# Kernel tuning notes

Measured on AMD Instinct MI355X. Metric: run time of the kernel, lower is better.

Reference implementation:

```python
import jax, jax.numpy as jnp
import numpy as np

B, T, D, H = 4, 2048, 384, 6
HD = D // H  # 64
HALF = HD // 2


def setup_inputs() -> dict:
    key = jax.random.key(0)
    k0, k1, k2 = jax.random.split(key, 3)
    x = jax.random.normal(k0, (B, T, D), jnp.float32)
    attn_bias = jnp.zeros((1, 1, T, T), jnp.float32)  # additive SDPA bias
    # standard RoPE tables: [T, HD/2]
    inv_freq = 1.0 / (10000.0 ** (np.arange(HALF, dtype=np.float32) / HALF))
    ang = np.arange(T, dtype=np.float32)[:, None] * inv_freq[None, :]
    cos = jnp.asarray(np.cos(ang), jnp.float32)
    sin = jnp.asarray(np.sin(ang), jnp.float32)
    w_qkv = jax.random.normal(k1, (D, 3 * D), jnp.float32) * (D ** -0.5)
    w_proj = jax.random.normal(k2, (D, D), jnp.float32) * (D ** -0.5)
    return {"x": x, "attn_bias": attn_bias, "cos": cos, "sin": sin,
            "w_qkv": w_qkv, "w_proj": w_proj}


def _apply_rope(x, cos, sin):
    # x: [b, h, t, hd]; cos/sin: [t, hd/2] -> rotate-half RoPE
    half = x.shape[-1] // 2
    x1, x2 = x[..., :half], x[..., half:]
    c = cos[None, None, :, :]
    s = sin[None, None, :, :]
    return jnp.concatenate([x1 * c - x2 * s, x2 * c + x1 * s], axis=-1)


def reference(x, attn_bias, cos, sin, w_qkv, w_proj):
    b, t, _ = x.shape
    qkv = (x @ w_qkv).reshape(b, t, 3, H, HD)  # fused QKV projection
    q = jnp.transpose(qkv[:, :, 0], (0, 2, 1, 3))  # [b,h,t,hd]
    k = jnp.transpose(qkv[:, :, 1], (0, 2, 1, 3))
    v = jnp.transpose(qkv[:, :, 2], (0, 2, 1, 3))
    q = _apply_rope(q, cos, sin)
    k = _apply_rope(k, cos, sin)
    scale = 1.0 / jnp.sqrt(jnp.asarray(HD, x.dtype))
    scores = jnp.einsum("bhqd,bhkd->bhqk", q, k) * scale + attn_bias
    attn = jax.nn.softmax(scores, axis=-1)
    out = jnp.einsum("bhqk,bhkd->bhqd", attn, v)
    out = jnp.transpose(out, (0, 2, 1, 3)).reshape(b, t, H * HD)
    return out @ w_proj
```

## Files before the change

### kernel.cpp

```cpp
#include <hip/hip_runtime.h>
#include <hip/hip_bf16.h>

#define BB   4
#define TT   2048
#define DDIM 384
#define HH   6
#define HD   64
#define BT   (BB*TT)
#define QKVC (3*DDIM)

typedef __attribute__((ext_vector_type(4))) short short4v;
typedef __attribute__((ext_vector_type(8))) short short8v;
typedef __attribute__((ext_vector_type(4))) float float4v;
typedef unsigned short u16;

static __device__ __forceinline__ u16 f2bu(float f) {
    __hip_bfloat16 h = __float2bfloat16(f);
    return __builtin_bit_cast(u16, h);
}

static __device__ __forceinline__ short8v ld_frag(const u16* p) {
    short4v a = *(const short4v*)p;
    short4v b = *(const short4v*)(p + 4);
    return __builtin_shufflevector(a, b, 0, 1, 2, 3, 4, 5, 6, 7);
}

static __device__ __forceinline__ void st8(u16* p, uint4 v) {
    *(uint2*)p       = make_uint2(v.x, v.y);
    *(uint2*)(p + 4) = make_uint2(v.z, v.w);
}

#define MFMA16(a, b, c) __builtin_amdgcn_mfma_f32_16x16x32_bf16((a), (b), (c), 0, 0, 0)

__global__ __launch_bounds__(256) void prep_kernel(
    const float* __restrict__ wqkv, const float* __restrict__ wproj,
    const float* __restrict__ x,
    u16* __restrict__ wqkvT, u16* __restrict__ wprojT, u16* __restrict__ xb)
{
    const int bid = blockIdx.x;
    const int t = threadIdx.x;
    if (bid >= 144) {
        size_t base = (size_t)(bid - 144) * 4096 + (size_t)t * 16;
        const float* gp = x + base;
        __align__(16) u16 tmp[16];
        #pragma unroll
        for (int u = 0; u < 4; ++u) {
            float4 v = *(const float4*)(gp + 4 * u);
            tmp[4 * u + 0] = f2bu(v.x); tmp[4 * u + 1] = f2bu(v.y);
            tmp[4 * u + 2] = f2bu(v.z); tmp[4 * u + 3] = f2bu(v.w);
        }
        *(uint4*)(xb + base)     = *(const uint4*)tmp;
        *(uint4*)(xb + base + 8) = *(const uint4*)(tmp + 8);
        return;
    }
    const float* in; u16* out; int K, C, c0, k0;
    if (bid < 108) { in = wqkv;  out = wqkvT;  K = DDIM; C = QKVC;
                     c0 = (bid % 18) * 64; k0 = (bid / 18) * 64; }
    else           { int b2 = bid - 108; in = wproj; out = wprojT; K = DDIM; C = DDIM;
                     c0 = (b2 % 6) * 64; k0 = (b2 / 6) * 64; }
    __shared__ float tr[64][65];
    {
        int kr = t >> 2, cb = (t & 3) * 16;
        const float* gp = in + (size_t)(k0 + kr) * C + c0 + cb;
        #pragma unroll
        for (int u = 0; u < 4; ++u) {
            float4 v = *(const float4*)(gp + 4 * u);
            tr[cb + 4 * u + 0][kr] = v.x;
            tr[cb + 4 * u + 1][kr] = v.y;
            tr[cb + 4 * u + 2][kr] = v.z;
            tr[cb + 4 * u + 3][kr] = v.w;
        }
    }
    __syncthreads();
    {
        int c = t >> 2, kb = (t & 3) * 16;
        __align__(16) u16 tmp[16];
        #pragma unroll
        for (int u = 0; u < 16; ++u) tmp[u] = f2bu(tr[c][kb + u]);
        u16* op = out + (size_t)(c0 + c) * K + k0 + kb;
        *(uint4*)op       = *(const uint4*)tmp;
        *(uint4*)(op + 8) = *(const uint4*)(tmp + 8);
    }
}

__global__ __launch_bounds__(256) void qkv_rope_kernel(
    const u16* __restrict__ xb, const u16* __restrict__ wt,
    const float* __restrict__ cs, const float* __restrict__ sn,
    u16* __restrict__ qb, u16* __restrict__ kb, u16* __restrict__ vtb)
{
    __shared__ __align__(16) u16 xs[2][64][68];
    __shared__ __align__(16) u16 ws[2][64][68];
    const int t = threadIdx.x;
    const int wv = t >> 6, lane = t & 63, quad = lane >> 4, lo = lane & 15;
    const int r0 = blockIdx.y * 64;
    const int c0 = blockIdx.x * 64;
    const int sr = t >> 3, sd = (t & 7) * 8;

    st8(&xs[0][sr][sd],      *(const uint4*)(xb + (size_t)(r0 + sr) * DDIM + sd));
    st8(&xs[0][sr + 32][sd], *(const uint4*)(xb + (size_t)(r0 + sr + 32) * DDIM + sd));
    st8(&ws[0][sr][sd],      *(const uint4*)(wt + (size_t)(c0 + sr) * DDIM + sd));
    st8(&ws[0][sr + 32][sd], *(const uint4*)(wt + (size_t)(c0 + sr + 32) * DDIM + sd));
    __syncthreads();

    float4v acc[4] = {};
    for (int kk = 0; kk < 6; ++kk) {
        const int cur = kk & 1, nxt = cur ^ 1;
        const int kkn = (kk < 5 ? kk + 1 : 5) * 64;
        uint4 xp0 = *(const uint4*)(xb + (size_t)(r0 + sr) * DDIM + kkn + sd);
        uint4 xp1 = *(const uint4*)(xb + (size_t)(r0 + sr + 32) * DDIM + kkn + sd);
        uint4 wp0 = *(const uint4*)(wt + (size_t)(c0 + sr) * DDIM + kkn + sd);
        uint4 wp1 = *(const uint4*)(wt + (size_t)(c0 + sr + 32) * DDIM + kkn + sd);

        #pragma unroll
        for (int kf = 0; kf < 2; ++kf) {
            short8v a = ld_frag(&xs[cur][16 * wv + lo][kf * 32 + quad * 8]);
            #pragma unroll
            for (int nt = 0; nt < 4; ++nt) {
                short8v b = ld_frag(&ws[cur][nt * 16 + lo][kf * 32 + quad * 8]);
                acc[nt] = MFMA16(a, b, acc[nt]);
            }
        }
        st8(&xs[nxt][sr][sd], xp0);
        st8(&xs[nxt][sr + 32][sd], xp1);
        st8(&ws[nxt][sr][sd], wp0);
        st8(&ws[nxt][sr + 32][sd], wp1);
        __syncthreads();
    }

    const int sec = blockIdx.x / 6;
    const int h   = blockIdx.x % 6;
    const int rbase = r0 + 16 * wv + 4 * quad;
    const int bidx  = r0 >> 11;
    const int tbase = rbase & (TT - 1);

    if (sec == 2) {
        #pragma unroll
        for (int nt = 0; nt < 4; ++nt) {
            int d = nt * 16 + lo;
            unsigned a0 = f2bu(acc[nt][0]) | ((unsigned)f2bu(acc[nt][1]) << 16);
            unsigned a1 = f2bu(acc[nt][2]) | ((unsigned)f2bu(acc[nt][3]) << 16);
            u16* gp = vtb + ((size_t)(bidx * HH + h) * HD + d) * TT + tbase;
            *(uint2*)gp = make_uint2(a0, a1);
        }
    } else {
        u16* dst = (sec == 0) ? qb : kb;
        #pragma unroll
        for (int np = 0; np < 2; ++np) {
            #pragma unroll
            for (int r = 0; r < 4; ++r) {
                int tpos = tbase + r;
                int ci = np * 16 + lo;
                float cv = cs[tpos * 32 + ci];
                float sv = sn[tpos * 32 + ci];
                float x1 = acc[np][r], x2 = acc[np + 2][r];
                u16* gp = dst + ((size_t)(bidx * HH + h) * TT + tpos) * HD;
                gp[ci]      = f2bu(x1 * cv - x2 * sv);
                gp[ci + 32] = f2bu(x2 * cv + x1 * sv);
            }
        }
    }
}

__global__ __launch_bounds__(256, 3) void attn_kernel(
    const u16* __restrict__ qb, const u16* __restrict__ kb, const u16* __restrict__ vtb,
    const float* __restrict__ bias, u16* __restrict__ ob)
{
    __shared__ __align__(16) u16 ks[2][64][68];
    __shared__ __align__(16) u16 vt[2][64][68];
    __shared__ __align__(16) u16 ps[4][16][72];

    const int t = threadIdx.x;
    const int wv = t >> 6, lane = t & 63, quad = lane >> 4, lo = lane & 15;
    const int bh = blockIdx.x;
    const int b = bh / HH, h = bh % HH;
    const int q0 = blockIdx.y * 64;
    const int qrow = q0 + 16 * wv + lo;

    const u16* qbase = qb + ((size_t)bh * TT + qrow) * HD + quad * 8;
    short8v aq0 = __builtin_bit_cast(short8v, *(const uint4*)qbase);
    short8v aq1 = __builtin_bit_cast(short8v, *(const uint4*)(qbase + 32));

    const int sr = t >> 3, sd = (t & 7) * 8;
    const u16* kbbase = kb + (size_t)bh * TT * HD;
    const u16* vtbase = vtb + (size_t)bh * HD * TT;
    const float* brow = bias + (size_t)qrow * TT + 4 * quad;

    st8(&ks[0][sr][sd],      *(const uint4*)(kbbase + (size_t)sr * HD + sd));
    st8(&ks[0][sr + 32][sd], *(const uint4*)(kbbase + (size_t)(sr + 32) * HD + sd));
    st8(&vt[0][sr][sd],      *(const uint4*)(vtbase + (size_t)sr * TT + sd));
    st8(&vt[0][sr + 32][sd], *(const uint4*)(vtbase + (size_t)(sr + 32) * TT + sd));
    float4 bcur[4];
    #pragma unroll
    for (int nt = 0; nt < 4; ++nt) bcur[nt] = *(const float4*)(brow + nt * 16);
    __syncthreads();

    float4v oacc[4] = {};
    float lacc[4] = {0.f, 0.f, 0.f, 0.f};

    for (int kt = 0; kt < TT / 64; ++kt) {
        const int cur = kt & 1, nxt = cur ^ 1;
        const int kn = (kt < 31 ? kt + 1 : 31) * 64;

        uint4 kp0 = *(const uint4*)(kbbase + (size_t)(kn + sr) * HD + sd);
        uint4 kp1 = *(const uint4*)(kbbase + (size_t)(kn + sr + 32) * HD + sd);
        uint4 vp0 = *(const uint4*)(vtbase + (size_t)sr * TT + kn + sd);
        uint4 vp1 = *(const uint4*)(vtbase + (size_t)(sr + 32) * TT + kn + sd);
        float4 bnxt[4];
        #pragma unroll
        for (int nt = 0; nt < 4; ++nt) bnxt[nt] = *(const float4*)(brow + kn + nt * 16);

        float4v s[4] = {};
        #pragma unroll
        for (int kf = 0; kf < 2; ++kf) {
            #pragma unroll
            for (int nt = 0; nt < 4; ++nt) {
                short8v kfr = ld_frag(&ks[cur][nt * 16 + lo][kf * 32 + quad * 8]);
                s[nt] = MFMA16(kfr, (kf ? aq1 : aq0), s[nt]);
            }
        }

        #pragma unroll
        for (int nt = 0; nt < 4; ++nt) {
            float p0 = __expf(fmaf(s[nt][0], 0.125f, bcur[nt].x));
            float p1 = __expf(fmaf(s[nt][1], 0.125f, bcur[nt].y));
            float p2 = __expf(fmaf(s[nt][2], 0.125f, bcur[nt].z));
            float p3 = __expf(fmaf(s[nt][3], 0.125f, bcur[nt].w));
            lacc[nt] += (p0 + p1) + (p2 + p3);
            short4v pv = { (short)f2bu(p0), (short)f2bu(p1),
                           (short)f2bu(p2), (short)f2bu(p3) };
            *(short4v*)&ps[wv][lo][nt * 16 + 4 * quad] = pv;
        }

        #pragma unroll
        for (int kf = 0; kf < 2; ++kf) {
            short8v ap = __builtin_bit_cast(short8v,
                *(const uint4*)&ps[wv][lo][kf * 32 + quad * 8]);
            #pragma unroll
            for (int dt = 0; dt < 4; ++dt) {
                short8v bv = ld_frag(&vt[cur][dt * 16 + lo][kf * 32 + quad * 8]);
                oacc[dt] = MFMA16(ap, bv, oacc[dt]);
            }
        }

        st8(&ks[nxt][sr][sd], kp0);
        st8(&ks[nxt][sr + 32][sd], kp1);
        st8(&vt[nxt][sr][sd], vp0);
        st8(&vt[nxt][sr + 32][sd], vp1);
        #pragma unroll
        for (int nt = 0; nt < 4; ++nt) bcur[nt] = bnxt[nt];
        __syncthreads();
    }

    float l = (lacc[0] + lacc[1]) + (lacc[2] + lacc[3]);
    l += __shfl_xor(l, 16);
    l += __shfl_xor(l, 32);
    #pragma unroll
    for (int r = 0; r < 4; ++r) {
        float lr = __shfl(l, 4 * quad + r);
        float inv = 1.f / lr;
        u16* gp = ob + ((size_t)b * TT + q0 + 16 * wv + 4 * quad + r) * DDIM + h * HD + lo;
        #pragma unroll
        for (int dt = 0; dt < 4; ++dt)
            gp[dt * 16] = f2bu(oacc[dt][r] * inv);
    }
}

__global__ __launch_bounds__(256) void proj_kernel(
    const u16* __restrict__ o, const u16* __restrict__ wt, float* __restrict__ out)
{
    __shared__ __align__(16) u16 os[2][64][68];
    __shared__ __align__(16) u16 ws[2][64][68];
    const int t = threadIdx.x;
    const int wv = t >> 6, lane = t & 63, quad = lane >> 4, lo = lane & 15;
    const int r0 = blockIdx.y * 64, c0 = blockIdx.x * 64;
    const int sr = t >> 3, sd = (t & 7) * 8;

    st8(&os[0][sr][sd],      *(const uint4*)(o + (size_t)(r0 + sr) * DDIM + sd));
    st8(&os[0][sr + 32][sd], *(const uint4*)(o + (size_t)(r0 + sr + 32) * DDIM + sd));
    st8(&ws[0][sr][sd],      *(const uint4*)(wt + (size_t)(c0 + sr) * DDIM + sd));
    st8(&ws[0][sr + 32][sd], *(const uint4*)(wt + (size_t)(c0 + sr + 32) * DDIM + sd));
    __syncthreads();

    float4v acc[4] = {};
    for (int kk = 0; kk < 6; ++kk) {
        const int cur = kk & 1, nxt = cur ^ 1;
        const int kkn = (kk < 5 ? kk + 1 : 5) * 64;
        uint4 op0 = *(const uint4*)(o + (size_t)(r0 + sr) * DDIM + kkn + sd);
        uint4 op1 = *(const uint4*)(o + (size_t)(r0 + sr + 32) * DDIM + kkn + sd);
        uint4 wp0 = *(const uint4*)(wt + (size_t)(c0 + sr) * DDIM + kkn + sd);
        uint4 wp1 = *(const uint4*)(wt + (size_t)(c0 + sr + 32) * DDIM + kkn + sd);

        #pragma unroll
        for (int kf = 0; kf < 2; ++kf) {
            short8v a = ld_frag(&os[cur][16 * wv + lo][kf * 32 + quad * 8]);
            #pragma unroll
            for (int nt = 0; nt < 4; ++nt) {
                short8v bfr = ld_frag(&ws[cur][nt * 16 + lo][kf * 32 + quad * 8]);
                acc[nt] = MFMA16(a, bfr, acc[nt]);
            }
        }
        st8(&os[nxt][sr][sd], op0);
        st8(&os[nxt][sr + 32][sd], op1);
        st8(&ws[nxt][sr][sd], wp0);
        st8(&ws[nxt][sr + 32][sd], wp1);
        __syncthreads();
    }
    #pragma unroll
    for (int r = 0; r < 4; ++r) {
        float* gp = out + (size_t)(r0 + 16 * wv + 4 * quad + r) * DDIM + c0;
        #pragma unroll
        for (int nt = 0; nt < 4; ++nt)
            gp[nt * 16 + lo] = acc[nt][r];
    }
}

extern "C" void kernel_launch(void* const* d_in, const int* in_sizes, int n_in,
                              void* d_out, int out_size, void* d_ws, size_t ws_size,
                              hipStream_t stream) {
    const float* x     = (const float*)d_in[0];
    const float* bias  = (const float*)d_in[1];
    const float* cs    = (const float*)d_in[2];
    const float* sn    = (const float*)d_in[3];
    const float* wqkv  = (const float*)d_in[4];
    const float* wproj = (const float*)d_in[5];
    float* out = (float*)d_out;

    u16* wqkvT  = (u16*)d_ws;
    u16* wprojT = wqkvT + (size_t)QKVC * DDIM;
    u16* qb     = wprojT + (size_t)DDIM * DDIM;
    u16* kb     = qb + (size_t)BB * HH * TT * HD;
    u16* vtb    = kb + (size_t)BB * HH * TT * HD;
    u16* ob     = vtb + (size_t)BB * HH * TT * HD;
    u16* xb     = ob + (size_t)BT * DDIM;

    prep_kernel<<<dim3(144 + BT * DDIM / 4096), 256, 0, stream>>>(
        wqkv, wproj, x, wqkvT, wprojT, xb);
    qkv_rope_kernel<<<dim3(QKVC / 64, BT / 64), 256, 0, stream>>>(
        xb, wqkvT, cs, sn, qb, kb, vtb);
    attn_kernel<<<dim3(BB * HH, TT / 64), 256, 0, stream>>>(qb, kb, vtb, bias, ob);
    proj_kernel<<<dim3(DDIM / 64, BT / 64), 256, 0, stream>>>(ob, wprojT, out);
}
```

Baseline: 176.5 us.

## Drop LDS staging; load MFMA fragments from global, exchange P via permlane swaps

All three GEMM-style kernels stop staging tiles through shared memory. Each lane now loads its MFMA fragments straight from global memory into registers, prefetches the next K step, and keeps a raw s_barrier to hold the waves in lockstep. In attention, the softmax P tile is rearranged into the A-operand layout with permlane32/16 swaps instead of an LDS round trip. The softmax scale and log2e are folded into Q during the RoPE epilogue so exp2 can be used directly. The cost is redundant global/L2 traffic, since each wave re-reads the shared K/V/weight tiles, plus higher register pressure after the occupancy hint is dropped.

```diff
diff --git a/kernel.cpp b/kernel.cpp
--- a/kernel.cpp
+++ b/kernel.cpp
@@ -9,7 +9,9 @@
 #define BT   (BB*TT)
 #define QKVC (3*DDIM)
 
-typedef __attribute__((ext_vector_type(4))) short short4v;
+#define QSCALE 0.18033688011112042f
+#define LOG2E  1.4426950408889634f
+
 typedef __attribute__((ext_vector_type(8))) short short8v;
 typedef __attribute__((ext_vector_type(4))) float float4v;
 typedef unsigned short u16;
@@ -18,16 +20,19 @@
     __hip_bfloat16 h = __float2bfloat16(f);
     return __builtin_bit_cast(u16, h);
 }
-
-static __device__ __forceinline__ short8v ld_frag(const u16* p) {
-    short4v a = *(const short4v*)p;
-    short4v b = *(const short4v*)(p + 4);
-    return __builtin_shufflevector(a, b, 0, 1, 2, 3, 4, 5, 6, 7);
-}
-
-static __device__ __forceinline__ void st8(u16* p, uint4 v) {
-    *(uint2*)p       = make_uint2(v.x, v.y);
-    *(uint2*)(p + 4) = make_uint2(v.z, v.w);
+static __device__ __forceinline__ unsigned pk2(float lo, float hi) {
+    return (unsigned)f2bu(lo) | ((unsigned)f2bu(hi) << 16);
+}
+static __device__ __forceinline__ short8v frag4(uint4 v) {
+    return __builtin_bit_cast(short8v, v);
+}
+static __device__ __forceinline__ void pl32swap(unsigned &a, unsigned &b) {
+    auto r = __builtin_amdgcn_permlane32_swap(a, b, false, false);
+    a = r[0]; b = r[1];
+}
+static __device__ __forceinline__ void pl16swap(unsigned &a, unsigned &b) {
+    auto r = __builtin_amdgcn_permlane16_swap(a, b, false, false);
+    a = r[0]; b = r[1];
 }
 
 #define MFMA16(a, b, c) __builtin_amdgcn_mfma_f32_16x16x32_bf16((a), (b), (c), 0, 0, 0)
@@ -88,43 +93,39 @@
     const float* __restrict__ cs, const float* __restrict__ sn,
     u16* __restrict__ qb, u16* __restrict__ kb, u16* __restrict__ vtb)
 {
-    __shared__ __align__(16) u16 xs[2][64][68];
-    __shared__ __align__(16) u16 ws[2][64][68];
     const int t = threadIdx.x;
     const int wv = t >> 6, lane = t & 63, quad = lane >> 4, lo = lane & 15;
-    const int r0 = blockIdx.y * 64;
-    const int c0 = blockIdx.x * 64;
-    const int sr = t >> 3, sd = (t & 7) * 8;
-
-    st8(&xs[0][sr][sd],      *(const uint4*)(xb + (size_t)(r0 + sr) * DDIM + sd));
-    st8(&xs[0][sr + 32][sd], *(const uint4*)(xb + (size_t)(r0 + sr + 32) * DDIM + sd));
-    st8(&ws[0][sr][sd],      *(const uint4*)(wt + (size_t)(c0 + sr) * DDIM + sd));
-    st8(&ws[0][sr + 32][sd], *(const uint4*)(wt + (size_t)(c0 + sr + 32) * DDIM + sd));
-    __syncthreads();
+    const int r0 = blockIdx.y * 64, c0 = blockIdx.x * 64;
+
+    const u16* abase = xb + (size_t)(r0 + 16 * wv + lo) * DDIM + quad * 8;
+    const u16* bbase = wt + (size_t)(c0 + lo) * DDIM + quad * 8;
+
+    uint4 af[2], bf[4][2];
+    af[0] = *(const uint4*)(abase);
+    af[1] = *(const uint4*)(abase + 32);
+    #pragma unroll
+    for (int nt = 0; nt < 4; ++nt) {
+        bf[nt][0] = *(const uint4*)(bbase + nt * 16 * DDIM);
+        bf[nt][1] = *(const uint4*)(bbase + nt * 16 * DDIM + 32);
+    }
 
     float4v acc[4] = {};
     for (int kk = 0; kk < 6; ++kk) {
-        const int cur = kk & 1, nxt = cur ^ 1;
-        const int kkn = (kk < 5 ? kk + 1 : 5) * 64;
-        uint4 xp0 = *(const uint4*)(xb + (size_t)(r0 + sr) * DDIM + kkn + sd);
-        uint4 xp1 = *(const uint4*)(xb + (size_t)(r0 + sr + 32) * DDIM + kkn + sd);
-        uint4 wp0 = *(const uint4*)(wt + (size_t)(c0 + sr) * DDIM + kkn + sd);
-        uint4 wp1 = *(const uint4*)(wt + (size_t)(c0 + sr + 32) * DDIM + kkn + sd);
-
-        #pragma unroll
-        for (int kf = 0; kf < 2; ++kf) {
-            short8v a = ld_frag(&xs[cur][16 * wv + lo][kf * 32 + quad * 8]);
-            #pragma unroll
-            for (int nt = 0; nt < 4; ++nt) {
-                short8v b = ld_frag(&ws[cur][nt * 16 + lo][kf * 32 + quad * 8]);
-                acc[nt] = MFMA16(a, b, acc[nt]);
-            }
-        }
-        st8(&xs[nxt][sr][sd], xp0);
-        st8(&xs[nxt][sr + 32][sd], xp1);
-        st8(&ws[nxt][sr][sd], wp0);
-        st8(&ws[nxt][sr + 32][sd], wp1);
-        __syncthreads();
+        __builtin_amdgcn_s_barrier();
+        const int kn = (kk < 5 ? kk + 1 : 5) * 64;
+        short8v a0 = frag4(af[0]), a1 = frag4(af[1]);
+        #pragma unroll
+        for (int nt = 0; nt < 4; ++nt) {
+            acc[nt] = MFMA16(a0, frag4(bf[nt][0]), acc[nt]);
+            acc[nt] = MFMA16(a1, frag4(bf[nt][1]), acc[nt]);
+        }
+        af[0] = *(const uint4*)(abase + kn);
+        af[1] = *(const uint4*)(abase + kn + 32);
+        #pragma unroll
+        for (int nt = 0; nt < 4; ++nt) {
+            bf[nt][0] = *(const uint4*)(bbase + nt * 16 * DDIM + kn);
+            bf[nt][1] = *(const uint4*)(bbase + nt * 16 * DDIM + kn + 32);
+        }
     }
 
     const int sec = blockIdx.x / 6;
@@ -137,13 +138,14 @@
         #pragma unroll
         for (int nt = 0; nt < 4; ++nt) {
             int d = nt * 16 + lo;
-            unsigned a0 = f2bu(acc[nt][0]) | ((unsigned)f2bu(acc[nt][1]) << 16);
-            unsigned a1 = f2bu(acc[nt][2]) | ((unsigned)f2bu(acc[nt][3]) << 16);
+            unsigned a0 = pk2(acc[nt][0], acc[nt][1]);
+            unsigned a1 = pk2(acc[nt][2], acc[nt][3]);
             u16* gp = vtb + ((size_t)(bidx * HH + h) * HD + d) * TT + tbase;
             *(uint2*)gp = make_uint2(a0, a1);
         }
     } else {
         u16* dst = (sec == 0) ? qb : kb;
+        const float scl = (sec == 0) ? QSCALE : 1.0f;
         #pragma unroll
         for (int np = 0; np < 2; ++np) {
             #pragma unroll
@@ -154,21 +156,17 @@
                 float sv = sn[tpos * 32 + ci];
                 float x1 = acc[np][r], x2 = acc[np + 2][r];
                 u16* gp = dst + ((size_t)(bidx * HH + h) * TT + tpos) * HD;
-                gp[ci]      = f2bu(x1 * cv - x2 * sv);
-                gp[ci + 32] = f2bu(x2 * cv + x1 * sv);
+                gp[ci]      = f2bu((x1 * cv - x2 * sv) * scl);
+                gp[ci + 32] = f2bu((x2 * cv + x1 * sv) * scl);
             }
         }
     }
 }
 
-__global__ __launch_bounds__(256, 3) void attn_kernel(
+__global__ __launch_bounds__(256) void attn_kernel(
     const u16* __restrict__ qb, const u16* __restrict__ kb, const u16* __restrict__ vtb,
     const float* __restrict__ bias, u16* __restrict__ ob)
 {
-    __shared__ __align__(16) u16 ks[2][64][68];
-    __shared__ __align__(16) u16 vt[2][64][68];
-    __shared__ __align__(16) u16 ps[4][16][72];
-
     const int t = threadIdx.x;
     const int wv = t >> 6, lane = t & 63, quad = lane >> 4, lo = lane & 15;
     const int bh = blockIdx.x;
@@ -177,78 +175,75 @@
     const int qrow = q0 + 16 * wv + lo;
 
     const u16* qbase = qb + ((size_t)bh * TT + qrow) * HD + quad * 8;
-    short8v aq0 = __builtin_bit_cast(short8v, *(const uint4*)qbase);
-    short8v aq1 = __builtin_bit_cast(short8v, *(const uint4*)(qbase + 32));
-
-    const int sr = t >> 3, sd = (t & 7) * 8;
-    const u16* kbbase = kb + (size_t)bh * TT * HD;
-    const u16* vtbase = vtb + (size_t)bh * HD * TT;
-    const float* brow = bias + (size_t)qrow * TT + 4 * quad;
-
-    st8(&ks[0][sr][sd],      *(const uint4*)(kbbase + (size_t)sr * HD + sd));
-    st8(&ks[0][sr + 32][sd], *(const uint4*)(kbbase + (size_t)(sr + 32) * HD + sd));
-    st8(&vt[0][sr][sd],      *(const uint4*)(vtbase + (size_t)sr * TT + sd));
-    st8(&vt[0][sr + 32][sd], *(const uint4*)(vtbase + (size_t)(sr + 32) * TT + sd));
-    float4 bcur[4];
-    #pragma unroll
-    for (int nt = 0; nt < 4; ++nt) bcur[nt] = *(const float4*)(brow + nt * 16);
-    __syncthreads();
+    short8v aq0 = frag4(*(const uint4*)qbase);
+    short8v aq1 = frag4(*(const uint4*)(qbase + 32));
+
+    const u16* kbase = kb + (size_t)bh * TT * HD + lo * HD + quad * 8;
+    const u16* vbase = vtb + (size_t)bh * HD * TT + lo * TT + quad * 8;
+    const float* bbase = bias + (size_t)qrow * TT + 4 * quad;
+
+    uint4 kq[4][2], vq[4][2];
+    float4 bc[4];
+    #pragma unroll
+    for (int nt = 0; nt < 4; ++nt) {
+        kq[nt][0] = *(const uint4*)(kbase + nt * 16 * HD);
+        kq[nt][1] = *(const uint4*)(kbase + nt * 16 * HD + 32);
+        vq[nt][0] = *(const uint4*)(vbase + nt * 16 * TT);
+        vq[nt][1] = *(const uint4*)(vbase + nt * 16 * TT + 32);
+        bc[nt]    = *(const float4*)(bbase + nt * 16);
+    }
 
     float4v oacc[4] = {};
     float lacc[4] = {0.f, 0.f, 0.f, 0.f};
 
     for (int kt = 0; kt < TT / 64; ++kt) {
-        const int cur = kt & 1, nxt = cur ^ 1;
-        const int kn = (kt < 31 ? kt + 1 : 31) * 64;
-
-        uint4 kp0 = *(const uint4*)(kbbase + (size_t)(kn + sr) * HD + sd);
-        uint4 kp1 = *(const uint4*)(kbbase + (size_t)(kn + sr + 32) * HD + sd);
-        uint4 vp0 = *(const uint4*)(vtbase + (size_t)sr * TT + kn + sd);
-        uint4 vp1 = *(const uint4*)(vtbase + (size_t)(sr + 32) * TT + kn + sd);
-        float4 bnxt[4];
-        #pragma unroll
-        for (int nt = 0; nt < 4; ++nt) bnxt[nt] = *(const float4*)(brow + kn + nt * 16);
+        __builtin_amdgcn_s_barrier();
+        const int kn = (kt < 31 ? kt + 1 : 31);
 
         float4v s[4] = {};
         #pragma unroll
-        for (int kf = 0; kf < 2; ++kf) {
-            #pragma unroll
-            for (int nt = 0; nt < 4; ++nt) {
-                short8v kfr = ld_frag(&ks[cur][nt * 16 + lo][kf * 32 + quad * 8]);
-                s[nt] = MFMA16(kfr, (kf ? aq1 : aq0), s[nt]);
-            }
-        }
-
-        #pragma unroll
-        for (int nt = 0; nt < 4; ++nt) {
-            float p0 = __expf(fmaf(s[nt][0], 0.125f, bcur[nt].x));
-            float p1 = __expf(fmaf(s[nt][1], 0.125f, bcur[nt].y));
-            float p2 = __expf(fmaf(s[nt][2], 0.125f, bcur[nt].z));
-            float p3 = __expf(fmaf(s[nt][3], 0.125f, bcur[nt].w));
+        for (int nt = 0; nt < 4; ++nt) {
+            s[nt] = MFMA16(frag4(kq[nt][0]), aq0, s[nt]);
+            s[nt] = MFMA16(frag4(kq[nt][1]), aq1, s[nt]);
+        }
+        #pragma unroll
+        for (int nt = 0; nt < 4; ++nt) {
+            kq[nt][0] = *(const uint4*)(kbase + kn * 64 * HD + nt * 16 * HD);
+            kq[nt][1] = *(const uint4*)(kbase + kn * 64 * HD + nt * 16 * HD + 32);
+        }
+
+        unsigned w[8];
+        #pragma unroll
+        for (int nt = 0; nt < 4; ++nt) {
+            float p0 = __builtin_amdgcn_exp2f(fmaf(bc[nt].x, LOG2E, s[nt][0]));
+            float p1 = __builtin_amdgcn_exp2f(fmaf(bc[nt].y, LOG2E, s[nt][1]));
+            float p2 = __builtin_amdgcn_exp2f(fmaf(bc[nt].z, LOG2E, s[nt][2]));
+            float p3 = __builtin_amdgcn_exp2f(fmaf(bc[nt].w, LOG2E, s[nt][3]));
             lacc[nt] += (p0 + p1) + (p2 + p3);
-            short4v pv = { (short)f2bu(p0), (short)f2bu(p1),
-                           (short)f2bu(p2), (short)f2bu(p3) };
-            *(short4v*)&ps[wv][lo][nt * 16 + 4 * quad] = pv;
-        }
-
-        #pragma unroll
-        for (int kf = 0; kf < 2; ++kf) {
-            short8v ap = __builtin_bit_cast(short8v,
-                *(const uint4*)&ps[wv][lo][kf * 32 + quad * 8]);
-            #pragma unroll
-            for (int dt = 0; dt < 4; ++dt) {
-                short8v bv = ld_frag(&vt[cur][dt * 16 + lo][kf * 32 + quad * 8]);
-                oacc[dt] = MFMA16(ap, bv, oacc[dt]);
-            }
-        }
-
-        st8(&ks[nxt][sr][sd], kp0);
-        st8(&ks[nxt][sr + 32][sd], kp1);
-        st8(&vt[nxt][sr][sd], vp0);
-        st8(&vt[nxt][sr + 32][sd], vp1);
-        #pragma unroll
-        for (int nt = 0; nt < 4; ++nt) bcur[nt] = bnxt[nt];
-        __syncthreads();
+            w[2 * nt]     = pk2(p0, p1);
+            w[2 * nt + 1] = pk2(p2, p3);
+        }
+        #pragma unroll
+        for (int nt = 0; nt < 4; ++nt)
+            bc[nt] = *(const float4*)(bbase + kn * 64 + nt * 16);
+
+        pl32swap(w[0], w[2]); pl16swap(w[0], w[2]);
+        pl32swap(w[1], w[3]); pl16swap(w[1], w[3]);
+        pl32swap(w[4], w[6]); pl16swap(w[4], w[6]);
+        pl32swap(w[5], w[7]); pl16swap(w[5], w[7]);
+        short8v pa0 = frag4(make_uint4(w[0], w[1], w[2], w[3]));
+        short8v pa1 = frag4(make_uint4(w[4], w[5], w[6], w[7]));
+
+        #pragma unroll
+        for (int dt = 0; dt < 4; ++dt) {
+            oacc[dt] = MFMA16(pa0, frag4(vq[dt][0]), oacc[dt]);
+            oacc[dt] = MFMA16(pa1, frag4(vq[dt][1]), oacc[dt]);
+        }
+        #pragma unroll
+        for (int dt = 0; dt < 4; ++dt) {
+            vq[dt][0] = *(const uint4*)(vbase + dt * 16 * TT + kn * 64);
+            vq[dt][1] = *(const uint4*)(vbase + dt * 16 * TT + kn * 64 + 32);
+        }
     }
 
     float l = (lacc[0] + lacc[1]) + (lacc[2] + lacc[3]);
@@ -268,42 +263,39 @@
 __global__ __launch_bounds__(256) void proj_kernel(
     const u16* __restrict__ o, const u16* __restrict__ wt, float* __restrict__ out)
 {
-    __shared__ __align__(16) u16 os[2][64][68];
-    __shared__ __align__(16) u16 ws[2][64][68];
     const int t = threadIdx.x;
     const int wv = t >> 6, lane = t & 63, quad = lane >> 4, lo = lane & 15;
     const int r0 = blockIdx.y * 64, c0 = blockIdx.x * 64;
-    const int sr = t >> 3, sd = (t & 7) * 8;
-
-    st8(&os[0][sr][sd],      *(const uint4*)(o + (size_t)(r0 + sr) * DDIM + sd));
-    st8(&os[0][sr + 32][sd], *(const uint4*)(o + (size_t)(r0 + sr + 32) * DDIM + sd));
-    st8(&ws[0][sr][sd],      *(const uint4*)(wt + (size_t)(c0 + sr) * DDIM + sd));
-    st8(&ws[0][sr + 32][sd], *(const uint4*)(wt + (size_t)(c0 + sr + 32) * DDIM + sd));
-    __syncthreads();
+
+    const u16* abase = o + (size_t)(r0 + 16 * wv + lo) * DDIM + quad * 8;
+    const u16* bbase = wt + (size_t)(c0 + lo) * DDIM + quad * 8;
+
+    uint4 af[2], bf[4][2];
+    af[0] = *(const uint4*)(abase);
+    af[1] = *(const uint4*)(abase + 32);
+    #pragma unroll
+    for (int nt = 0; nt < 4; ++nt) {
+        bf[nt][0] = *(const uint4*)(bbase + nt * 16 * DDIM);
+        bf[nt][1] = *(const uint4*)(bbase + nt * 16 * DDIM + 32);
+    }
 
     float4v acc[4] = {};
     for (int kk = 0; kk < 6; ++kk) {
-        const int cur = kk & 1, nxt = cur ^ 1;
-        const int kkn = (kk < 5 ? kk + 1 : 5) * 64;
-        uint4 op0 = *(const uint4*)(o + (size_t)(r0 + sr) * DDIM + kkn + sd);
-        uint4 op1 = *(const uint4*)(o + (size_t)(r0 + sr + 32) * DDIM + kkn + sd);
-        uint4 wp0 = *(const uint4*)(wt + (size_t)(c0 + sr) * DDIM + kkn + sd);
-        uint4 wp1 = *(const uint4*)(wt + (size_t)(c0 + sr + 32) * DDIM + kkn + sd);
-
-        #pragma unroll
-        for (int kf = 0; kf < 2; ++kf) {
-            short8v a = ld_frag(&os[cur][16 * wv + lo][kf * 32 + quad * 8]);
-            #pragma unroll
-            for (int nt = 0; nt < 4; ++nt) {
-                short8v bfr = ld_frag(&ws[cur][nt * 16 + lo][kf * 32 + quad * 8]);
-                acc[nt] = MFMA16(a, bfr, acc[nt]);
-            }
-        }
-        st8(&os[nxt][sr][sd], op0);
-        st8(&os[nxt][sr + 32][sd], op1);
-        st8(&ws[nxt][sr][sd], wp0);
-        st8(&ws[nxt][sr + 32][sd], wp1);
-        __syncthreads();
+        __builtin_amdgcn_s_barrier();
+        const int kn = (kk < 5 ? kk + 1 : 5) * 64;
+        short8v a0 = frag4(af[0]), a1 = frag4(af[1]);
+        #pragma unroll
+        for (int nt = 0; nt < 4; ++nt) {
+            acc[nt] = MFMA16(a0, frag4(bf[nt][0]), acc[nt]);
+            acc[nt] = MFMA16(a1, frag4(bf[nt][1]), acc[nt]);
+        }
+        af[0] = *(const uint4*)(abase + kn);
+        af[1] = *(const uint4*)(abase + kn + 32);
+        #pragma unroll
+        for (int nt = 0; nt < 4; ++nt) {
+            bf[nt][0] = *(const uint4*)(bbase + nt * 16 * DDIM + kn);
+            bf[nt][1] = *(const uint4*)(bbase + nt * 16 * DDIM + kn + 32);
+        }
     }
     #pragma unroll
     for (int r = 0; r < 4; ++r) {
```

After: 386.3 us. 119% more time.

## Keep P in registers via permlane swaps, fold scale into Q, bf16 bias

Applied to the files above, without the earlier changes.

Attention no longer stages the probability tile through shared memory. It repacks P into MFMA A-fragments with permlane32/16 swaps, which removes the LDS round-trip and frees shared memory, and occupancy is raised to 4 blocks. The softmax scale and log2e are folded into Q during RoPE so exp2 can be used directly. The bias is pre-converted to bf16 (times log2e) in the prep kernel when workspace allows, halving bias traffic but adding a 2048x2048 conversion pass and bf16 rounding of the bias. s_setprio is also wrapped around the MFMA sections.

```diff
diff --git a/kernel.cpp b/kernel.cpp
--- a/kernel.cpp
+++ b/kernel.cpp
@@ -9,6 +9,9 @@
 #define BT   (BB*TT)
 #define QKVC (3*DDIM)
 
+#define QSCALE 0.18033688011112042f
+#define LOG2E  1.4426950408889634f
+
 typedef __attribute__((ext_vector_type(4))) short short4v;
 typedef __attribute__((ext_vector_type(8))) short short8v;
 typedef __attribute__((ext_vector_type(4))) float float4v;
@@ -18,39 +21,62 @@
     __hip_bfloat16 h = __float2bfloat16(f);
     return __builtin_bit_cast(u16, h);
 }
-
+static __device__ __forceinline__ unsigned pk2(float lo, float hi) {
+    return (unsigned)f2bu(lo) | ((unsigned)f2bu(hi) << 16);
+}
+static __device__ __forceinline__ float bu2f_lo(unsigned u) {
+    return __builtin_bit_cast(float, u << 16);
+}
+static __device__ __forceinline__ float bu2f_hi(unsigned u) {
+    return __builtin_bit_cast(float, u & 0xffff0000u);
+}
+static __device__ __forceinline__ short8v frag4(uint4 v) {
+    return __builtin_bit_cast(short8v, v);
+}
 static __device__ __forceinline__ short8v ld_frag(const u16* p) {
     short4v a = *(const short4v*)p;
     short4v b = *(const short4v*)(p + 4);
     return __builtin_shufflevector(a, b, 0, 1, 2, 3, 4, 5, 6, 7);
 }
-
 static __device__ __forceinline__ void st8(u16* p, uint4 v) {
     *(uint2*)p       = make_uint2(v.x, v.y);
     *(uint2*)(p + 4) = make_uint2(v.z, v.w);
 }
+static __device__ __forceinline__ void pl32swap(unsigned &a, unsigned &b) {
+    auto r = __builtin_amdgcn_permlane32_swap(a, b, false, false);
+    a = r[0]; b = r[1];
+}
+static __device__ __forceinline__ void pl16swap(unsigned &a, unsigned &b) {
+    auto r = __builtin_amdgcn_permlane16_swap(a, b, false, false);
+    a = r[0]; b = r[1];
+}
 
 #define MFMA16(a, b, c) __builtin_amdgcn_mfma_f32_16x16x32_bf16((a), (b), (c), 0, 0, 0)
 
 __global__ __launch_bounds__(256) void prep_kernel(
     const float* __restrict__ wqkv, const float* __restrict__ wproj,
-    const float* __restrict__ x,
-    u16* __restrict__ wqkvT, u16* __restrict__ wprojT, u16* __restrict__ xb)
+    const float* __restrict__ x, const float* __restrict__ bias,
+    u16* __restrict__ wqkvT, u16* __restrict__ wprojT,
+    u16* __restrict__ xb, u16* __restrict__ bias16)
 {
     const int bid = blockIdx.x;
     const int t = threadIdx.x;
     if (bid >= 144) {
-        size_t base = (size_t)(bid - 144) * 4096 + (size_t)t * 16;
-        const float* gp = x + base;
+        const float* src; u16* dst; float scl; size_t base;
+        if (bid < 912) { src = x;    dst = xb;     scl = 1.0f;
+                         base = (size_t)(bid - 144) * 4096 + (size_t)t * 16; }
+        else           { src = bias; dst = bias16; scl = LOG2E;
+                         base = (size_t)(bid - 912) * 4096 + (size_t)t * 16; }
+        const float* gp = src + base;
         __align__(16) u16 tmp[16];
         #pragma unroll
         for (int u = 0; u < 4; ++u) {
             float4 v = *(const float4*)(gp + 4 * u);
-            tmp[4 * u + 0] = f2bu(v.x); tmp[4 * u + 1] = f2bu(v.y);
-            tmp[4 * u + 2] = f2bu(v.z); tmp[4 * u + 3] = f2bu(v.w);
-        }
-        *(uint4*)(xb + base)     = *(const uint4*)tmp;
-        *(uint4*)(xb + base + 8) = *(const uint4*)(tmp + 8);
+            tmp[4 * u + 0] = f2bu(v.x * scl); tmp[4 * u + 1] = f2bu(v.y * scl);
+            tmp[4 * u + 2] = f2bu(v.z * scl); tmp[4 * u + 3] = f2bu(v.w * scl);
+        }
+        *(uint4*)(dst + base)     = *(const uint4*)tmp;
+        *(uint4*)(dst + base + 8) = *(const uint4*)(tmp + 8);
         return;
     }
     const float* in; u16* out; int K, C, c0, k0;
@@ -137,13 +163,14 @@
         #pragma unroll
         for (int nt = 0; nt < 4; ++nt) {
             int d = nt * 16 + lo;
-            unsigned a0 = f2bu(acc[nt][0]) | ((unsigned)f2bu(acc[nt][1]) << 16);
-            unsigned a1 = f2bu(acc[nt][2]) | ((unsigned)f2bu(acc[nt][3]) << 16);
+            unsigned a0 = pk2(acc[nt][0], acc[nt][1]);
+            unsigned a1 = pk2(acc[nt][2], acc[nt][3]);
             u16* gp = vtb + ((size_t)(bidx * HH + h) * HD + d) * TT + tbase;
             *(uint2*)gp = make_uint2(a0, a1);
         }
     } else {
         u16* dst = (sec == 0) ? qb : kb;
+        const float scl = (sec == 0) ? QSCALE : 1.0f;
         #pragma unroll
         for (int np = 0; np < 2; ++np) {
             #pragma unroll
@@ -154,20 +181,21 @@
                 float sv = sn[tpos * 32 + ci];
                 float x1 = acc[np][r], x2 = acc[np + 2][r];
                 u16* gp = dst + ((size_t)(bidx * HH + h) * TT + tpos) * HD;
-                gp[ci]      = f2bu(x1 * cv - x2 * sv);
-                gp[ci + 32] = f2bu(x2 * cv + x1 * sv);
-            }
-        }
-    }
-}
-
-__global__ __launch_bounds__(256, 3) void attn_kernel(
+                gp[ci]      = f2bu((x1 * cv - x2 * sv) * scl);
+                gp[ci + 32] = f2bu((x2 * cv + x1 * sv) * scl);
+            }
+        }
+    }
+}
+
+template <bool B16>
+__global__ __launch_bounds__(256, 4) void attn_kernel(
     const u16* __restrict__ qb, const u16* __restrict__ kb, const u16* __restrict__ vtb,
-    const float* __restrict__ bias, u16* __restrict__ ob)
+    const float* __restrict__ bias, const u16* __restrict__ bias16,
+    u16* __restrict__ ob)
 {
     __shared__ __align__(16) u16 ks[2][64][68];
     __shared__ __align__(16) u16 vt[2][64][68];
-    __shared__ __align__(16) u16 ps[4][16][72];
 
     const int t = threadIdx.x;
     const int wv = t >> 6, lane = t & 63, quad = lane >> 4, lo = lane & 15;
@@ -177,21 +205,25 @@
     const int qrow = q0 + 16 * wv + lo;
 
     const u16* qbase = qb + ((size_t)bh * TT + qrow) * HD + quad * 8;
-    short8v aq0 = __builtin_bit_cast(short8v, *(const uint4*)qbase);
-    short8v aq1 = __builtin_bit_cast(short8v, *(const uint4*)(qbase + 32));
+    short8v aq0 = frag4(*(const uint4*)qbase);
+    short8v aq1 = frag4(*(const uint4*)(qbase + 32));
 
     const int sr = t >> 3, sd = (t & 7) * 8;
     const u16* kbbase = kb + (size_t)bh * TT * HD;
     const u16* vtbase = vtb + (size_t)bh * HD * TT;
     const float* brow = bias + (size_t)qrow * TT + 4 * quad;
+    const u16* brow16 = bias16 + (size_t)qrow * TT + 4 * quad;
 
     st8(&ks[0][sr][sd],      *(const uint4*)(kbbase + (size_t)sr * HD + sd));
     st8(&ks[0][sr + 32][sd], *(const uint4*)(kbbase + (size_t)(sr + 32) * HD + sd));
     st8(&vt[0][sr][sd],      *(const uint4*)(vtbase + (size_t)sr * TT + sd));
     st8(&vt[0][sr + 32][sd], *(const uint4*)(vtbase + (size_t)(sr + 32) * TT + sd));
-    float4 bcur[4];
+    float4 bcur[4]; uint2 bcur16[4];
     #pragma unroll
-    for (int nt = 0; nt < 4; ++nt) bcur[nt] = *(const float4*)(brow + nt * 16);
+    for (int nt = 0; nt < 4; ++nt) {
+        if constexpr (B16) bcur16[nt] = *(const uint2*)(brow16 + nt * 16);
+        else               bcur[nt]   = *(const float4*)(brow + nt * 16);
+    }
     __syncthreads();
 
     float4v oacc[4] = {};
@@ -205,11 +237,15 @@
         uint4 kp1 = *(const uint4*)(kbbase + (size_t)(kn + sr + 32) * HD + sd);
         uint4 vp0 = *(const uint4*)(vtbase + (size_t)sr * TT + kn + sd);
         uint4 vp1 = *(const uint4*)(vtbase + (size_t)(sr + 32) * TT + kn + sd);
-        float4 bnxt[4];
-        #pragma unroll
-        for (int nt = 0; nt < 4; ++nt) bnxt[nt] = *(const float4*)(brow + kn + nt * 16);
+        float4 bnxt[4]; uint2 bnxt16[4];
+        #pragma unroll
+        for (int nt = 0; nt < 4; ++nt) {
+            if constexpr (B16) bnxt16[nt] = *(const uint2*)(brow16 + kn + nt * 16);
+            else               bnxt[nt]   = *(const float4*)(brow + kn + nt * 16);
+        }
 
         float4v s[4] = {};
+        __builtin_amdgcn_s_setprio(1);
         #pragma unroll
         for (int kf = 0; kf < 2; ++kf) {
             #pragma unroll
@@ -218,36 +254,55 @@
                 s[nt] = MFMA16(kfr, (kf ? aq1 : aq0), s[nt]);
             }
         }
-
+        __builtin_amdgcn_s_setprio(0);
+
+        unsigned w[8];
         #pragma unroll
         for (int nt = 0; nt < 4; ++nt) {
-            float p0 = __expf(fmaf(s[nt][0], 0.125f, bcur[nt].x));
-            float p1 = __expf(fmaf(s[nt][1], 0.125f, bcur[nt].y));
-            float p2 = __expf(fmaf(s[nt][2], 0.125f, bcur[nt].z));
-            float p3 = __expf(fmaf(s[nt][3], 0.125f, bcur[nt].w));
+            float b0, b1, b2, b3;
+            if constexpr (B16) {
+                b0 = bu2f_lo(bcur16[nt].x); b1 = bu2f_hi(bcur16[nt].x);
+                b2 = bu2f_lo(bcur16[nt].y); b3 = bu2f_hi(bcur16[nt].y);
+            } else {
+                b0 = bcur[nt].x * LOG2E; b1 = bcur[nt].y * LOG2E;
+                b2 = bcur[nt].z * LOG2E; b3 = bcur[nt].w * LOG2E;
+            }
+            float p0 = __builtin_amdgcn_exp2f(s[nt][0] + b0);
+            float p1 = __builtin_amdgcn_exp2f(s[nt][1] + b1);
+            float p2 = __builtin_amdgcn_exp2f(s[nt][2] + b2);
+            float p3 = __builtin_amdgcn_exp2f(s[nt][3] + b3);
             lacc[nt] += (p0 + p1) + (p2 + p3);
-            short4v pv = { (short)f2bu(p0), (short)f2bu(p1),
-                           (short)f2bu(p2), (short)f2bu(p3) };
-            *(short4v*)&ps[wv][lo][nt * 16 + 4 * quad] = pv;
-        }
-
+            w[2 * nt]     = pk2(p0, p1);
+            w[2 * nt + 1] = pk2(p2, p3);
+        }
+
+        pl32swap(w[0], w[2]); pl16swap(w[0], w[2]);
+        pl32swap(w[1], w[3]); pl16swap(w[1], w[3]);
+        pl32swap(w[4], w[6]); pl16swap(w[4], w[6]);
+        pl32swap(w[5], w[7]); pl16swap(w[5], w[7]);
+        short8v pa0 = frag4(make_uint4(w[0], w[1], w[2], w[3]));
+        short8v pa1 = frag4(make_uint4(w[4], w[5], w[6], w[7]));
+
+        __builtin_amdgcn_s_setprio(1);
         #pragma unroll
         for (int kf = 0; kf < 2; ++kf) {
-            short8v ap = __builtin_bit_cast(short8v,
-                *(const uint4*)&ps[wv][lo][kf * 32 + quad * 8]);
             #pragma unroll
             for (int dt = 0; dt < 4; ++dt) {
                 short8v bv = ld_frag(&vt[cur][dt * 16 + lo][kf * 32 + quad * 8]);
-                oacc[dt] = MFMA16(ap, bv, oacc[dt]);
-            }
-        }
+                oacc[dt] = MFMA16((kf ? pa1 : pa0), bv, oacc[dt]);
+            }
+        }
+        __builtin_amdgcn_s_setprio(0);
 
         st8(&ks[nxt][sr][sd], kp0);
         st8(&ks[nxt][sr + 32][sd], kp1);
         st8(&vt[nxt][sr][sd], vp0);
         st8(&vt[nxt][sr + 32][sd], vp1);
         #pragma unroll
-        for (int nt = 0; nt < 4; ++nt) bcur[nt] = bnxt[nt];
+        for (int nt = 0; nt < 4; ++nt) {
+            if constexpr (B16) bcur16[nt] = bnxt16[nt];
+            else               bcur[nt]   = bnxt[nt];
+        }
         __syncthreads();
     }
 
@@ -332,11 +387,20 @@
     u16* vtb    = kb + (size_t)BB * HH * TT * HD;
     u16* ob     = vtb + (size_t)BB * HH * TT * HD;
     u16* xb     = ob + (size_t)BT * DDIM;
-
-    prep_kernel<<<dim3(144 + BT * DDIM / 4096), 256, 0, stream>>>(
-        wqkv, wproj, x, wqkvT, wprojT, xb);
+    u16* bias16 = xb + (size_t)BT * DDIM;
+
+    const size_t need_b16 = ((size_t)(bias16 - wqkvT) + (size_t)TT * TT) * sizeof(u16);
+    const bool useb16 = ws_size >= need_b16;
+
+    prep_kernel<<<dim3(144 + BT * DDIM / 4096 + (useb16 ? TT * TT / 4096 : 0)),
+                  256, 0, stream>>>(wqkv, wproj, x, bias, wqkvT, wprojT, xb, bias16);
     qkv_rope_kernel<<<dim3(QKVC / 64, BT / 64), 256, 0, stream>>>(
         xb, wqkvT, cs, sn, qb, kb, vtb);
-    attn_kernel<<<dim3(BB * HH, TT / 64), 256, 0, stream>>>(qb, kb, vtb, bias, ob);
+    if (useb16)
+        attn_kernel<true><<<dim3(BB * HH, TT / 64), 256, 0, stream>>>(
+            qb, kb, vtb, bias, bias16, ob);
+    else
+        attn_kernel<false><<<dim3(BB * HH, TT / 64), 256, 0, stream>>>(
+            qb, kb, vtb, bias, bias16, ob);
     proj_kernel<<<dim3(DDIM / 64, BT / 64), 256, 0, stream>>>(ob, wprojT, out);
 }
```

Result: no change. 179.8 us (+1.9%).
